# Kernel tuning notes

Measured on AMD Instinct MI355X. Metric: run time of the kernel, lower is better.

Reference implementation:

```python
import jax, jax.numpy as jnp
import numpy as np
from jax.scipy.special import gammaln

N_TIMES = 131072
MAX_ITER = 4
DAMPING = 0.5
PREC_FLOOR = 1e-6
DEG = 20
TWO_PI = 2.0 * np.pi


def _gh_nodes(deg):
    # Nodes/weights such that sum(w * g(m + s*x)) = E_{N(m, s^2)}[g]
    xh, wh = np.polynomial.hermite.hermgauss(deg)
    x = np.sqrt(2.0) * xh
    w = wh / np.sqrt(np.pi)
    return jnp.asarray(x, jnp.float32), jnp.asarray(w, jnp.float32)


def _discretise_matern32(times, lam, sigma2):
    # dt_full = [0, diff(times)]; first step keeps the stationary prior.
    dt = jnp.concatenate([jnp.zeros((1,), times.dtype), jnp.diff(times)])
    ld = lam * dt
    e = jnp.exp(-ld)
    row0 = jnp.stack([1.0 + ld, dt], axis=-1)            # [N,2]
    row1 = jnp.stack([-(lam ** 2) * dt, 1.0 - ld], axis=-1)
    A = e[:, None, None] * jnp.stack([row0, row1], axis=-2)  # [N,2,2]
    P_inf = jnp.diag(jnp.stack([sigma2, (lam ** 2) * sigma2]))  # [2,2]
    Q = P_inf[None] - jnp.einsum('nij,jk,nlk->nil', A, P_inf, A)
    return A, Q, P_inf


def _kalman_filter(A_seq, Q_seq, P_inf, residual, mask, R_seq):
    # Scalar observation model with H = [1, 0].
    d = A_seq.shape[-1]
    def step(carry, inp):
        m, P, ll = carry
        A, Q, r, mk, R = inp
        m_pred = A @ m
        P_pred = A @ P @ A.T + Q
        v = r - m_pred[0]
        S = P_pred[0, 0] + R
        K = P_pred[:, 0] / S                      # Kalman gain [d]
        m_f = m_pred + mk * v * K
        P_f = P_pred - mk * S * jnp.outer(K, K)
        ll = ll - 0.5 * mk * (jnp.log(TWO_PI * S) + v * v / S)
        return (m_f, P_f, ll), (m_pred, P_pred, m_f, P_f)
    init = (jnp.zeros((d,), A_seq.dtype), P_inf, jnp.zeros((), A_seq.dtype))
    (_, _, log_marg), (m_pred, P_pred, m_filt, P_filt) = jax.lax.scan(
        step, init, (A_seq, Q_seq, residual, mask, R_seq))
    return m_pred, P_pred, m_filt, P_filt, log_marg


def _rts_smoother(m_pred, P_pred, m_filt, P_filt, A_seq):
    def step(carry, inp):
        ms_next, Ps_next = carry
        m_f, P_f, A_n, m_p, P_p = inp   # A_n, m_p, P_p are at step n+1
        # G = P_f A^T P_p^{-1}  (P_p symmetric)
        G = jnp.linalg.solve(P_p, A_n @ P_f).T
        ms = m_f + G @ (ms_next - m_p)
        Ps = P_f + G @ (Ps_next - P_p) @ G.T
        return (ms, Ps), (ms, Ps)
    init = (m_filt[-1], P_filt[-1])
    inputs = (m_filt[:-1], P_filt[:-1], A_seq[1:], m_pred[1:], P_pred[1:])
    _, (ms, Ps) = jax.lax.scan(step, init, inputs, reverse=True)
    m_s = jnp.concatenate([ms, m_filt[-1:]], axis=0)
    P_s = jnp.concatenate([Ps, P_filt[-1:]], axis=0)
    return m_s, P_s


def _smoothed_posterior(times, lam, sigma2, nat1, nat2):
    A, Q, P_inf = _discretise_matern32(times, lam, sigma2)
    R_seq = jnp.reciprocal(nat2)
    residual = nat1 / nat2          # prior mean is zero
    mask = jnp.ones_like(times)
    m_pred, P_pred, m_filt, P_filt, log_marg = _kalman_filter(
        A, Q, P_inf, residual, mask, R_seq)
    m_s, P_s = _rts_smoother(m_pred, P_pred, m_filt, P_filt, A)
    f_mean = m_s[:, 0]
    f_var = jnp.maximum(P_s[:, 0, 0], 1e-12)
    return f_mean, f_var, log_marg


def _log_prob(f, y):
    # Poisson likelihood with exp link, per scalar point.
    return y * f - jnp.exp(f) - gammaln(y + 1.0)


def setup_inputs() -> dict:
    key = jax.random.key(0)
    k1, k2 = jax.random.split(key)
    times = jnp.sort(jax.random.uniform(k1, (N_TIMES,), jnp.float32, 0.0, 1000.0))
    y = jax.random.randint(k2, (N_TIMES,), 0, 10, dtype=jnp.int32)
    return {
        'times': times,
        'y': y,
        'log_lengthscale': jnp.zeros((1,), jnp.float32),
        'log_variance': jnp.zeros((1,), jnp.float32),
    }


def reference(times, y, log_lengthscale, log_variance):
    y_f = y.astype(times.dtype)
    ell = jnp.exp(log_lengthscale[0])
    sigma2 = jnp.exp(log_variance[0])
    lam = jnp.sqrt(3.0) / ell
    x_nodes, w_nodes = _gh_nodes(DEG)
    N = times.shape[0]

    grad_fn = jax.vmap(jax.vmap(jax.grad(_log_prob)))           # [deg,N]
    hess_fn = jax.vmap(jax.vmap(jax.grad(jax.grad(_log_prob))))
    y_b = jnp.broadcast_to(y_f, (DEG, N))

    nat1 = jnp.zeros((N,), times.dtype)
    nat2 = jnp.full((N,), PREC_FLOOR, times.dtype)
    q_mean = jnp.zeros((N,), times.dtype)   # prior mean
    q_var = jnp.ones((N,), times.dtype)

    for _ in range(MAX_ITER):
        cav_prec = jnp.maximum(jnp.reciprocal(q_var) - nat2, PREC_FLOOR)
        cav_var = jnp.reciprocal(cav_prec)
        cav_mean = cav_var * (q_mean / q_var - nat1)
        f_grid = cav_mean[None, :] + jnp.sqrt(cav_var)[None, :] * x_nodes[:, None]
        g_avg = jnp.einsum('k,kn->n', w_nodes, grad_fn(f_grid, y_b))
        h_avg = jnp.einsum('k,kn->n', w_nodes, hess_fn(f_grid, y_b))
        new_prec = jnp.maximum(-h_avg, PREC_FLOOR)
        new_nat1 = g_avg + new_prec * cav_mean
        nat1 = (1.0 - DAMPING) * nat1 + DAMPING * new_nat1
        nat2 = jnp.maximum((1.0 - DAMPING) * nat2 + DAMPING * new_prec, PREC_FLOOR)
        q_mean, q_var, _ = _smoothed_posterior(times, lam, sigma2, nat1, nat2)

    return q_mean
```

## Files before the change

### kernel.cpp

```cpp
#include <hip/hip_runtime.h>
#include <math.h>

#define BLK   384
#define EPT   2
#define WIN   (BLK*EPT)
#define CHUNK 512
#define HALO  128
#define NW    (BLK/64)

typedef float v2f __attribute__((ext_vector_type(2)));

__device__ __forceinline__ float frcp(float x){ return __builtin_amdgcn_rcpf(x); }
__device__ __forceinline__ v2f mkv2(float x, float y){ v2f r; r.x=x; r.y=y; return r; }

struct FT { v2f A0,A1,b,C0,C1,e,J0,J1; };
struct ST { v2f E0,E1,g,L0,L1; };
struct BC { v2f b,C0,C1; };
struct GL { v2f g,L0,L1; };

template<int CTRL, typename T>
__device__ __forceinline__ T dpp_mov(const T& v){
  T r; const int* s=(const int*)&v; int* p=(int*)&r;
  constexpr int n = sizeof(T)/4;
  #pragma unroll
  for (int i=0;i<n;i++)
    p[i] = __builtin_amdgcn_update_dpp(s[i], s[i], CTRL, 0xf, 0xf, false);
  return r;
}
template<typename T>
__device__ __forceinline__ T shflup(const T& v, int d){
  T r; const float* s=(const float*)&v; float* p=(float*)&r;
  constexpr int n = sizeof(T)/4;
  #pragma unroll
  for (int i=0;i<n;i++) p[i] = __shfl_up(s[i], (unsigned)d, 64);
  return r;
}
template<typename T>
__device__ __forceinline__ T shflrev(const T& v, int revl){
  T r; const float* s=(const float*)&v; float* p=(float*)&r;
  constexpr int n = sizeof(T)/4;
  #pragma unroll
  for (int i=0;i<n;i++) p[i] = __shfl(s[i], revl, 64);
  return r;
}
template<typename T>
__device__ __forceinline__ void lds_store(float (*arr)[NW], int col, const T& v){
  const float* s=(const float*)&v;
  constexpr int n = sizeof(T)/4;
  #pragma unroll
  for (int i=0;i<n;i++) arr[i][col] = s[i];
}
template<typename T>
__device__ __forceinline__ T lds_load(const float (*arr)[NW], int col){
  T r; float* p=(float*)&r;
  constexpr int n = sizeof(T)/4;
  #pragma unroll
  for (int i=0;i<n;i++) p[i] = arr[i][col];
  return r;
}

__device__ __forceinline__ FT comb_f(const FT& a, const FT& b){
  FT o;
  v2f T0 = a.C0.x*b.J0 + a.C0.y*b.J1; T0.x += 1.f;
  v2f T1 = a.C1.x*b.J0 + a.C1.y*b.J1; T1.y += 1.f;
  const float idet = frcp(T0.x*T1.y - T0.y*T1.x);
  const v2f M0 = idet * mkv2( T1.y, -T0.y);
  const v2f M1 = idet * mkv2(-T1.x,  T0.x);
  const v2f P0 = b.A0.x*M0 + b.A0.y*M1;
  const v2f P1 = b.A1.x*M0 + b.A1.y*M1;
  o.A0 = P0.x*a.A0 + P0.y*a.A1;
  o.A1 = P1.x*a.A0 + P1.y*a.A1;
  const v2f u = a.b + b.e.x*a.C0 + b.e.y*a.C1;
  o.b = mkv2(P0.x*u.x + P0.y*u.y + b.b.x,
             P1.x*u.x + P1.y*u.y + b.b.y);
  const v2f W0 = P0.x*a.C0 + P0.y*a.C1;
  const v2f W1 = P1.x*a.C0 + P1.y*a.C1;
  const float c00 = W0.x*b.A0.x + W0.y*b.A0.y + b.C0.x;
  const float c01 = W0.x*b.A1.x + W0.y*b.A1.y + b.C0.y;
  const float c11 = W1.x*b.A1.x + W1.y*b.A1.y + b.C1.y;
  o.C0 = mkv2(c00,c01); o.C1 = mkv2(c01,c11);
  const v2f v = b.e - (a.b.x*b.J0 + a.b.y*b.J1);
  const v2f Nv = v.x*M0 + v.y*M1;
  o.e = a.e + Nv.x*a.A0 + Nv.y*a.A1;
  const v2f X0 = M0.x*b.J0 + M1.x*b.J1;
  const v2f X1 = M0.y*b.J0 + M1.y*b.J1;
  const v2f Y0 = a.A0.x*X0 + a.A1.x*X1;
  const v2f Y1 = a.A0.y*X0 + a.A1.y*X1;
  const float j00 = Y0.x*a.A0.x + Y0.y*a.A1.x + a.J0.x;
  const float j01 = Y0.x*a.A0.y + Y0.y*a.A1.y + a.J0.y;
  const float j11 = Y1.x*a.A0.y + Y1.y*a.A1.y + a.J1.y;
  o.J0 = mkv2(j00,j01); o.J1 = mkv2(j01,j11);
  return o;
}

__device__ __forceinline__ BC comb_bc(const BC& a, const FT& b){
  BC o;
  v2f T0 = a.C0.x*b.J0 + a.C0.y*b.J1; T0.x += 1.f;
  v2f T1 = a.C1.x*b.J0 + a.C1.y*b.J1; T1.y += 1.f;
  const float idet = frcp(T0.x*T1.y - T0.y*T1.x);
  const v2f M0 = idet * mkv2( T1.y, -T0.y);
  const v2f M1 = idet * mkv2(-T1.x,  T0.x);
  const v2f P0 = b.A0.x*M0 + b.A0.y*M1;
  const v2f P1 = b.A1.x*M0 + b.A1.y*M1;
  const v2f u = a.b + b.e.x*a.C0 + b.e.y*a.C1;
  o.b = mkv2(P0.x*u.x + P0.y*u.y + b.b.x,
             P1.x*u.x + P1.y*u.y + b.b.y);
  const v2f W0 = P0.x*a.C0 + P0.y*a.C1;
  const v2f W1 = P1.x*a.C0 + P1.y*a.C1;
  const float c00 = W0.x*b.A0.x + W0.y*b.A0.y + b.C0.x;
  const float c01 = W0.x*b.A1.x + W0.y*b.A1.y + b.C0.y;
  const float c11 = W1.x*b.A1.x + W1.y*b.A1.y + b.C1.y;
  o.C0 = mkv2(c00,c01); o.C1 = mkv2(c01,c11);
  return o;
}

__device__ __forceinline__ ST comb_s(const ST& a, const ST& b){
  ST o;
  o.E0 = b.E0.x*a.E0 + b.E0.y*a.E1;
  o.E1 = b.E1.x*a.E0 + b.E1.y*a.E1;
  o.g = mkv2(b.E0.x*a.g.x + b.E0.y*a.g.y + b.g.x,
             b.E1.x*a.g.x + b.E1.y*a.g.y + b.g.y);
  const v2f W0 = b.E0.x*a.L0 + b.E0.y*a.L1;
  const v2f W1 = b.E1.x*a.L0 + b.E1.y*a.L1;
  const float l00 = W0.x*b.E0.x + W0.y*b.E0.y + b.L0.x;
  const float l01 = W0.x*b.E1.x + W0.y*b.E1.y + b.L0.y;
  const float l11 = W1.x*b.E1.x + W1.y*b.E1.y + b.L1.y;
  o.L0 = mkv2(l00,l01); o.L1 = mkv2(l01,l11);
  return o;
}
__device__ __forceinline__ GL comb_gl(const GL& a, const ST& b){
  GL o;
  o.g = mkv2(b.E0.x*a.g.x + b.E0.y*a.g.y + b.g.x,
             b.E1.x*a.g.x + b.E1.y*a.g.y + b.g.y);
  const v2f W0 = b.E0.x*a.L0 + b.E0.y*a.L1;
  const v2f W1 = b.E1.x*a.L0 + b.E1.y*a.L1;
  const float l00 = W0.x*b.E0.x + W0.y*b.E0.y + b.L0.x;
  const float l01 = W0.x*b.E1.x + W0.y*b.E1.y + b.L0.y;
  const float l11 = W1.x*b.E1.x + W1.y*b.E1.y + b.L1.y;
  o.L0 = mkv2(l00,l01); o.L1 = mkv2(l01,l11);
  return o;
}

__device__ __forceinline__ void compute_fq(double dt, double lam, double s2,
    v2f& F0, v2f& F1, v2f& Q0, v2f& Q1){
  const double ld = lam*dt, e = exp(-ld), e2 = e*e;
  F0 = mkv2((float)(e*(1.0+ld)), (float)(e*dt));
  F1 = mkv2((float)(-lam*lam*dt*e), (float)(e*(1.0-ld)));
  const float q00 = (float)(s2*(1.0 - e2*((1.0+ld)*(1.0+ld)+ld*ld)));
  const float q01 = (float)(2.0*s2*lam*e2*ld*ld);
  const float q11 = (float)(lam*lam*s2*(1.0 - e2*(ld*ld+(1.0-ld)*(1.0-ld))));
  Q0 = mkv2(q00,q01); Q1 = mkv2(q01,q11);
}

__device__ __forceinline__ FT build_felem(bool prior,
    const v2f F0, const v2f F1, const v2f Q0, const v2f Q1,
    float n1, float n2, float sigma2, float lam2s2)
{
  FT e;
  const float R = frcp(n2);
  const float yy = n1*R;
  if (prior){
    e.A0 = mkv2(0.f,0.f); e.A1 = mkv2(0.f,0.f);
    const float K0 = sigma2*frcp(sigma2 + R);
    e.b = mkv2(K0*yy, 0.f);
    e.C0 = mkv2(sigma2 - K0*sigma2, 0.f); e.C1 = mkv2(0.f, lam2s2);
    e.e = mkv2(0.f,0.f); e.J0 = mkv2(0.f,0.f); e.J1 = mkv2(0.f,0.f);
  } else {
    const float iS = frcp(Q0.x + R);
    const float K0 = Q0.x*iS, K1 = Q0.y*iS;
    const float om = 1.f - K0;
    e.A0 = om*F0;
    e.A1 = F1 - K1*F0;
    e.b = mkv2(K0*yy, K1*yy);
    e.C0 = om*Q0;
    e.C1 = mkv2(e.C0.y, Q1.y - K1*Q0.y);
    e.e = (yy*iS)*F0;
    e.J0 = (iS*F0.x)*F0;
    e.J1 = mkv2(e.J0.y, iS*F0.y*F0.y);
  }
  return e;
}

__device__ __forceinline__ ST build_selem(const v2f m, const v2f Pf0, const v2f Pf1,
    const v2f F0, const v2f F1, const v2f Q0, const v2f Q1)
{
  ST e;
  const v2f W0 = F0.x*Pf0 + F0.y*Pf1;
  const v2f W1 = F1.x*Pf0 + F1.y*Pf1;
  const float Pp00 = W0.x*F0.x + W0.y*F0.y + Q0.x;
  const float Pp01 = W0.x*F1.x + W0.y*F1.y + Q0.y;
  const float Pp11 = W1.x*F1.x + W1.y*F1.y + Q1.y;
  const float idet = frcp(Pp00*Pp11 - Pp01*Pp01);
  const v2f Pi0 = idet * mkv2( Pp11, -Pp01);
  const v2f Pi1 = idet * mkv2(-Pp01,  Pp00);
  e.E0 = W0.x*Pi0 + W1.x*Pi1;
  e.E1 = W0.y*Pi0 + W1.y*Pi1;
  const float mp0 = F0.x*m.x + F0.y*m.y;
  const float mp1 = F1.x*m.x + F1.y*m.y;
  e.g = mkv2(m.x - (e.E0.x*mp0 + e.E0.y*mp1),
             m.y - (e.E1.x*mp0 + e.E1.y*mp1));
  const v2f Ppr0 = mkv2(Pp00,Pp01), Ppr1 = mkv2(Pp01,Pp11);
  const v2f Z0 = e.E0.x*Ppr0 + e.E0.y*Ppr1;
  const v2f Z1 = e.E1.x*Ppr0 + e.E1.y*Ppr1;
  const float l00 = Pf0.x - (Z0.x*e.E0.x + Z0.y*e.E0.y);
  const float l01 = Pf0.y - (Z0.x*e.E1.x + Z0.y*e.E1.y);
  const float l11 = Pf1.y - (Z1.x*e.E1.x + Z1.y*e.E1.y);
  e.L0 = mkv2(l00,l01); e.L1 = mkv2(l01,l11);
  return e;
}

__global__ __launch_bounds__(BLK, 1) void fused_kernel(
    const float* __restrict__ times, const int* __restrict__ y,
    const float* __restrict__ ll, const float* __restrict__ lv,
    float* __restrict__ out, int N)
{
  __shared__ float shF[16][NW];
  __shared__ float shS[10][NW];

  const int t = threadIdx.x, b = blockIdx.x;
  const int lane = t & 63, w = t >> 6;
  const int revl = 63 - lane;
  const int cs = b * CHUNK;
  int ws = cs - HALO;
  if (ws < 0) ws = 0;
  if (ws > N - WIN) ws = N - WIN;
  const int g0 = ws + t * EPT;

  const double lamd    = sqrt(3.0)/exp((double)ll[0]);
  const double sigma2d = exp((double)lv[0]);
  const float sigma2 = (float)sigma2d;
  const float lam2s2 = (float)(lamd*lamd*sigma2d);

  v2f aF0[EPT+1], aF1[EPT+1], aQ0[EPT+1], aQ1[EPT+1];
  {
    const float tprev = (g0 > 0) ? times[g0-1] : 0.f;
    const float2 tv = *(const float2*)(times + g0);
    const float tnx = (g0+2 <= N-1) ? times[g0+2] : times[N-1];
    compute_fq((g0==0) ? 0.0 : ((double)tv.x-(double)tprev), lamd, sigma2d, aF0[0],aF1[0],aQ0[0],aQ1[0]);
    compute_fq((double)tv.y-(double)tv.x, lamd, sigma2d, aF0[1],aF1[1],aQ0[1],aQ1[1]);
    compute_fq((double)tnx-(double)tv.y, lamd, sigma2d, aF0[2],aF1[2],aQ0[2],aQ1[2]);
  }
  float yf[EPT];
  {
    const int2 yv = *(const int2*)(y + g0);
    yf[0]=(float)yv.x; yf[1]=(float)yv.y;
  }

  float nat1[EPT], nat2[EPT], qm[EPT], qv[EPT];
  #pragma unroll
  for (int c=0;c<EPT;c++){ nat1[c]=0.f; nat2[c]=1e-6f; qm[c]=0.f; qv[c]=1.f; }

  const bool priorElem = (t == 0);
  const bool lastThr   = (t == BLK-1);

  for (int it=0; it<4; ++it){
    #pragma unroll
    for (int c=0;c<EPT;c++){
      const float iqv = frcp(qv[c]);
      const float cp = fmaxf(iqv - nat2[c], 1e-6f);
      const float cv = frcp(cp);
      const float cm = cv*(qm[c]*iqv - nat1[c]);
      const float Ee = __expf(cm + 0.5f*cv);
      const float np  = fmaxf(Ee, 1e-6f);
      const float nn1 = (yf[c] - Ee) + np*cm;
      nat1[c] = 0.5f*nat1[c] + 0.5f*nn1;
      nat2[c] = fmaxf(0.5f*nat2[c] + 0.5f*np, 1e-6f);
    }

    FT part0 = build_felem(priorElem, aF0[0],aF1[0],aQ0[0],aQ1[0],
                           nat1[0], nat2[0], sigma2, lam2s2);
    FT part1;
    {
      const FT e1 = build_felem(false, aF0[1],aF1[1],aQ0[1],aQ1[1],
                                nat1[1], nat2[1], sigma2, lam2s2);
      part1 = comb_f(part0, e1);
    }
    FT acc = part1;
    { const FT p = dpp_mov<0x111>(acc); if ((lane&15)>=1) acc = comb_f(p, acc); }
    { const FT p = dpp_mov<0x112>(acc); if ((lane&15)>=2) acc = comb_f(p, acc); }
    { const FT p = dpp_mov<0x114>(acc); if ((lane&15)>=4) acc = comb_f(p, acc); }
    { const FT p = dpp_mov<0x118>(acc); if ((lane&15)>=8) acc = comb_f(p, acc); }
    { const FT p = dpp_mov<0x142>(acc); if (lane & 16)    acc = comb_f(p, acc); }
    { const FT p = dpp_mov<0x143>(acc); if (lane >= 32)   acc = comb_f(p, acc); }
    if (lane == 63) lds_store(shF, w, acc);
    __syncthreads();
    BC pre; pre.b=mkv2(0.f,0.f); pre.C0=mkv2(0.f,0.f); pre.C1=mkv2(0.f,0.f);
    for (int j=0; j<w; ++j){
      const FT a = lds_load<FT>(shF, j);
      pre = comb_bc(pre, a);
    }
    {
      const FT lex = shflup(acc, 1);
      if (lane > 0) pre = comb_bc(pre, lex);
    }
    v2f mv[EPT], Pr0[EPT], Pr1[EPT];
    {
      const BC r0 = comb_bc(pre, part0);
      const BC r1 = comb_bc(pre, part1);
      mv[0]=r0.b; Pr0[0]=r0.C0; Pr1[0]=r0.C1;
      mv[1]=r1.b; Pr0[1]=r1.C0; Pr1[1]=r1.C1;
    }

    const int rw = NW-1-w;
    ST spart1;
    if (lastThr){
      spart1.E0 = mkv2(0.f,0.f); spart1.E1 = mkv2(0.f,0.f);
      spart1.g = mv[1]; spart1.L0 = Pr0[1]; spart1.L1 = Pr1[1];
    } else {
      spart1 = build_selem(mv[1], Pr0[1], Pr1[1], aF0[2],aF1[2],aQ0[2],aQ1[2]);
    }
    ST spart0;
    {
      const ST e0 = build_selem(mv[0], Pr0[0], Pr1[0], aF0[1],aF1[1],aQ0[1],aQ1[1]);
      spart0 = comb_s(spart1, e0);
    }
    const ST sflip0 = shflrev(spart0, revl);
    const ST sflip1 = shflrev(spart1, revl);
    ST sacc = sflip0;
    { const ST p = dpp_mov<0x111>(sacc); if ((lane&15)>=1) sacc = comb_s(p, sacc); }
    { const ST p = dpp_mov<0x112>(sacc); if ((lane&15)>=2) sacc = comb_s(p, sacc); }
    { const ST p = dpp_mov<0x114>(sacc); if ((lane&15)>=4) sacc = comb_s(p, sacc); }
    { const ST p = dpp_mov<0x118>(sacc); if ((lane&15)>=8) sacc = comb_s(p, sacc); }
    { const ST p = dpp_mov<0x142>(sacc); if (lane & 16)    sacc = comb_s(p, sacc); }
    { const ST p = dpp_mov<0x143>(sacc); if (lane >= 32)   sacc = comb_s(p, sacc); }
    if (lane == 63) lds_store(shS, rw, sacc);
    __syncthreads();
    GL spre; spre.g=mkv2(0.f,0.f); spre.L0=mkv2(0.f,0.f); spre.L1=mkv2(0.f,0.f);
    for (int j=0; j<rw; ++j){
      const ST a = lds_load<ST>(shS, j);
      spre = comb_gl(spre, a);
    }
    {
      const ST slex = shflup(sacc, 1);
      if (lane > 0) spre = comb_gl(spre, slex);
    }
    {
      const GL r0 = comb_gl(spre, sflip0);
      const GL r1 = comb_gl(spre, sflip1);
      qm[0] = __shfl(r0.g.x, revl, 64);
      qv[0] = fmaxf(__shfl(r0.L0.x, revl, 64), 1e-12f);
      qm[1] = __shfl(r1.g.x, revl, 64);
      qv[1] = fmaxf(__shfl(r1.L0.x, revl, 64), 1e-12f);
    }

    if (it == 3){
      if (g0 >= cs && g0 + EPT <= cs + CHUNK){
        float2 o; o.x=qm[0]; o.y=qm[1];
        *(float2*)(out + g0) = o;
      }
    }
  }
}

extern "C" void kernel_launch(void* const* d_in, const int* in_sizes, int n_in,
                              void* d_out, int out_size, void* d_ws, size_t ws_size,
                              hipStream_t stream) {
  (void)n_in; (void)out_size; (void)d_ws; (void)ws_size;
  const int N = in_sizes[0];
  const float* times = (const float*)d_in[0];
  const int*   y     = (const int*)d_in[1];
  const float* ll    = (const float*)d_in[2];
  const float* lv    = (const float*)d_in[3];
  float* out = (float*)d_out;

  const int G = N / CHUNK;
  fused_kernel<<<G, BLK, 0, stream>>>(times, y, ll, lv, out, N);
}
```

Baseline: 34.39 us.

## Use 512-thread blocks with mixed two-element and one-element threads

The block grows from 384 to 512 threads while the 768-element window stays the same. The first 256 threads each handle two elements and the remaining 256 handle one. This shortens the sequential per-thread work and adds more warps for latency hiding. In exchange there is an extra cross-warp prefix step through LDS, divergent branches on the heavy flag, and scalar loads and stores replacing the vectorised ones.

```diff
diff --git a/kernel.cpp b/kernel.cpp
--- a/kernel.cpp
+++ b/kernel.cpp
@@ -1,9 +1,8 @@
 #include <hip/hip_runtime.h>
 #include <math.h>
 
-#define BLK   384
-#define EPT   2
-#define WIN   (BLK*EPT)
+#define BLK   512
+#define WIN   768
 #define CHUNK 512
 #define HALO  128
 #define NW    (BLK/64)
@@ -220,42 +219,47 @@
   const int t = threadIdx.x, b = blockIdx.x;
   const int lane = t & 63, w = t >> 6;
   const int revl = 63 - lane;
+  const bool heavy = (t < 256);
   const int cs = b * CHUNK;
   int ws = cs - HALO;
   if (ws < 0) ws = 0;
   if (ws > N - WIN) ws = N - WIN;
-  const int g0 = ws + t * EPT;
+  const int g0 = heavy ? (ws + 2*t) : (ws + 256 + t);
 
   const double lamd    = sqrt(3.0)/exp((double)ll[0]);
   const double sigma2d = exp((double)lv[0]);
   const float sigma2 = (float)sigma2d;
   const float lam2s2 = (float)(lamd*lamd*sigma2d);
 
-  v2f aF0[EPT+1], aF1[EPT+1], aQ0[EPT+1], aQ1[EPT+1];
+  v2f aF0[3], aF1[3], aQ0[3], aQ1[3];
   {
-    const float tprev = (g0 > 0) ? times[g0-1] : 0.f;
-    const float2 tv = *(const float2*)(times + g0);
-    const float tnx = (g0+2 <= N-1) ? times[g0+2] : times[N-1];
-    compute_fq((g0==0) ? 0.0 : ((double)tv.x-(double)tprev), lamd, sigma2d, aF0[0],aF1[0],aQ0[0],aQ1[0]);
-    compute_fq((double)tv.y-(double)tv.x, lamd, sigma2d, aF0[1],aF1[1],aQ0[1],aQ1[1]);
-    compute_fq((double)tnx-(double)tv.y, lamd, sigma2d, aF0[2],aF1[2],aQ0[2],aQ1[2]);
+    const float tm1 = (g0 > 0) ? times[g0-1] : 0.f;
+    const float t0 = times[g0];
+    const float t1 = (g0+1 <= N-1) ? times[g0+1] : t0;
+    compute_fq((g0==0) ? 0.0 : ((double)t0-(double)tm1), lamd, sigma2d,
+               aF0[0],aF1[0],aQ0[0],aQ1[0]);
+    compute_fq((double)t1-(double)t0, lamd, sigma2d,
+               aF0[1],aF1[1],aQ0[1],aQ1[1]);
+    if (heavy){
+      const float t2 = times[g0+2];
+      compute_fq((double)t2-(double)t1, lamd, sigma2d,
+                 aF0[2],aF1[2],aQ0[2],aQ1[2]);
+    }
   }
-  float yf[EPT];
-  {
-    const int2 yv = *(const int2*)(y + g0);
-    yf[0]=(float)yv.x; yf[1]=(float)yv.y;
-  }
-
-  float nat1[EPT], nat2[EPT], qm[EPT], qv[EPT];
-  #pragma unroll
-  for (int c=0;c<EPT;c++){ nat1[c]=0.f; nat2[c]=1e-6f; qm[c]=0.f; qv[c]=1.f; }
+  float yf[2];
+  yf[0] = (float)y[g0];
+  yf[1] = heavy ? (float)y[g0+1] : 0.f;
+
+  float nat1[2], nat2[2], qm[2], qv[2];
+  #pragma unroll
+  for (int c=0;c<2;c++){ nat1[c]=0.f; nat2[c]=1e-6f; qm[c]=0.f; qv[c]=1.f; }
 
   const bool priorElem = (t == 0);
   const bool lastThr   = (t == BLK-1);
 
   for (int it=0; it<4; ++it){
-    #pragma unroll
-    for (int c=0;c<EPT;c++){
+    const int nc = heavy ? 2 : 1;
+    for (int c=0;c<nc;c++){
       const float iqv = frcp(qv[c]);
       const float cp = fmaxf(iqv - nat2[c], 1e-6f);
       const float cv = frcp(cp);
@@ -270,10 +274,12 @@
     FT part0 = build_felem(priorElem, aF0[0],aF1[0],aQ0[0],aQ1[0],
                            nat1[0], nat2[0], sigma2, lam2s2);
     FT part1;
-    {
+    if (heavy){
       const FT e1 = build_felem(false, aF0[1],aF1[1],aQ0[1],aQ1[1],
                                 nat1[1], nat2[1], sigma2, lam2s2);
       part1 = comb_f(part0, e1);
+    } else {
+      part1 = part0;
     }
     FT acc = part1;
     { const FT p = dpp_mov<0x111>(acc); if ((lane&15)>=1) acc = comb_f(p, acc); }
@@ -293,29 +299,32 @@
       const FT lex = shflup(acc, 1);
       if (lane > 0) pre = comb_bc(pre, lex);
     }
-    v2f mv[EPT], Pr0[EPT], Pr1[EPT];
+    v2f mv[2], Pr0[2], Pr1[2];
     {
       const BC r0 = comb_bc(pre, part0);
-      const BC r1 = comb_bc(pre, part1);
       mv[0]=r0.b; Pr0[0]=r0.C0; Pr1[0]=r0.C1;
-      mv[1]=r1.b; Pr0[1]=r1.C0; Pr1[1]=r1.C1;
+      if (heavy){
+        const BC r1 = comb_bc(pre, part1);
+        mv[1]=r1.b; Pr0[1]=r1.C0; Pr1[1]=r1.C1;
+      }
     }
 
     const int rw = NW-1-w;
-    ST spart1;
-    if (lastThr){
-      spart1.E0 = mkv2(0.f,0.f); spart1.E1 = mkv2(0.f,0.f);
-      spart1.g = mv[1]; spart1.L0 = Pr0[1]; spart1.L1 = Pr1[1];
-    } else {
+    ST spart0, spart1;
+    if (heavy){
       spart1 = build_selem(mv[1], Pr0[1], Pr1[1], aF0[2],aF1[2],aQ0[2],aQ1[2]);
-    }
-    ST spart0;
-    {
       const ST e0 = build_selem(mv[0], Pr0[0], Pr1[0], aF0[1],aF1[1],aQ0[1],aQ1[1]);
       spart0 = comb_s(spart1, e0);
+    } else {
+      if (lastThr){
+        spart0.E0 = mkv2(0.f,0.f); spart0.E1 = mkv2(0.f,0.f);
+        spart0.g = mv[0]; spart0.L0 = Pr0[0]; spart0.L1 = Pr1[0];
+      } else {
+        spart0 = build_selem(mv[0], Pr0[0], Pr1[0], aF0[1],aF1[1],aQ0[1],aQ1[1]);
+      }
+      spart1 = spart0;
     }
     const ST sflip0 = shflrev(spart0, revl);
-    const ST sflip1 = shflrev(spart1, revl);
     ST sacc = sflip0;
     { const ST p = dpp_mov<0x111>(sacc); if ((lane&15)>=1) sacc = comb_s(p, sacc); }
     { const ST p = dpp_mov<0x112>(sacc); if ((lane&15)>=2) sacc = comb_s(p, sacc); }
@@ -336,18 +345,19 @@
     }
     {
       const GL r0 = comb_gl(spre, sflip0);
-      const GL r1 = comb_gl(spre, sflip1);
       qm[0] = __shfl(r0.g.x, revl, 64);
       qv[0] = fmaxf(__shfl(r0.L0.x, revl, 64), 1e-12f);
-      qm[1] = __shfl(r1.g.x, revl, 64);
-      qv[1] = fmaxf(__shfl(r1.L0.x, revl, 64), 1e-12f);
+      if (heavy){
+        const ST sflip1 = shflrev(spart1, revl);
+        const GL r1 = comb_gl(spre, sflip1);
+        qm[1] = __shfl(r1.g.x, revl, 64);
+        qv[1] = fmaxf(__shfl(r1.L0.x, revl, 64), 1e-12f);
+      }
     }
 
     if (it == 3){
-      if (g0 >= cs && g0 + EPT <= cs + CHUNK){
-        float2 o; o.x=qm[0]; o.y=qm[1];
-        *(float2*)(out + g0) = o;
-      }
+      if (g0 >= cs && g0 < cs + CHUNK) out[g0] = qm[0];
+      if (heavy && (g0+1 >= cs && g0+1 < cs + CHUNK)) out[g0+1] = qm[1];
     }
   }
 }
```

Result: slower. 36.05 us (+4.8%).
